# Optimization experiments

Hardware: AMD Instinct MI355X
Metric: run time of the kernel (lower is better)

Reference implementation:

```python
import jax, jax.numpy as jnp
import numpy as np

N = 50000
E = 800000
F_IN = 500
H = 5          # heads
C = 32         # per-head channels
HID = H * C    # 160
NC = 20        # num_classes
G = 8          # number of graphs in batch
SLOPE_ATT = 0.2   # GATConv attention leaky slope (PyG default)
SLOPE_ACT = 0.01  # F.leaky_relu default


def _layernorm(x, scale, bias, eps=1e-5):
    mu = jnp.mean(x, axis=-1, keepdims=True)
    var = jnp.var(x, axis=-1, keepdims=True)
    return (x - mu) * jax.lax.rsqrt(var + eps) * scale + bias


def _edge_softmax(logits, dst, num_nodes):
    # segment softmax over incoming edges of each destination node
    m = jax.ops.segment_max(logits, dst, num_segments=num_nodes)
    ex = jnp.exp(logits - m[dst])
    s = jax.ops.segment_sum(ex, dst, num_segments=num_nodes)
    return ex / (s[dst] + 1e-16)


def _gat_layer(x, src, dst, W, a_src, a_dst, b):
    n = x.shape[0]
    h = (x @ W).reshape(n, H, C)                       # [N,H,C]
    al_s = jnp.einsum('nhc,hc->nh', h, a_src)          # [N,H]
    al_d = jnp.einsum('nhc,hc->nh', h, a_dst)
    logits = jax.nn.leaky_relu(al_s[src] + al_d[dst], SLOPE_ATT)  # [Et,H]
    alpha = _edge_softmax(logits, dst, n)              # [Et,H]
    msg = h[src] * alpha[..., None]                    # [Et,H,C]
    out = jax.ops.segment_sum(msg, dst, num_segments=n).reshape(n, HID) + b
    return out, alpha


def setup_inputs():
    key = jax.random.key(0)
    ks = jax.random.split(key, 24)
    p = lambda k, shp: jax.random.normal(k, shp, jnp.float32) * 0.05
    x = jax.random.normal(ks[0], (N, F_IN), jnp.float32)
    edge_index = jax.random.randint(ks[1], (2, E), 0, N, jnp.int64)
    batch = jnp.sort(jax.random.randint(ks[2], (N,), 0, G, jnp.int64))
    return {
        'x': x, 'edge_index': edge_index, 'batch': batch,
        'W1': p(ks[3], (F_IN, HID)), 'a_src1': p(ks[4], (H, C)), 'a_dst1': p(ks[5], (H, C)), 'b1': jnp.zeros((HID,), jnp.float32),
        'ln1_s': jnp.ones((HID,), jnp.float32), 'ln1_b': jnp.zeros((HID,), jnp.float32),
        'W2': p(ks[6], (HID, HID)), 'a_src2': p(ks[7], (H, C)), 'a_dst2': p(ks[8], (H, C)), 'b2': jnp.zeros((HID,), jnp.float32),
        'ln2_s': jnp.ones((HID,), jnp.float32), 'ln2_b': jnp.zeros((HID,), jnp.float32),
        'Wm': p(ks[9], (HID, HID)), 'bm': jnp.zeros((HID,), jnp.float32),
        'Wmlp1': p(ks[10], (HID, HID)), 'bmlp1': jnp.zeros((HID,), jnp.float32),
        'ln3_s': jnp.ones((HID,), jnp.float32), 'ln3_b': jnp.zeros((HID,), jnp.float32),
        'Wmlp2': p(ks[11], (HID, NC)), 'bmlp2': jnp.zeros((NC,), jnp.float32),
    }


def reference(x, edge_index, batch, W1, a_src1, a_dst1, b1, ln1_s, ln1_b,
              W2, a_src2, a_dst2, b2, ln2_s, ln2_b, Wm, bm,
              Wmlp1, bmlp1, ln3_s, ln3_b, Wmlp2, bmlp2):
    n = x.shape[0]
    # PyG GATConv adds self-loops by default
    loops = jnp.arange(n, dtype=edge_index.dtype)
    src = jnp.concatenate([edge_index[0], loops])
    dst = jnp.concatenate([edge_index[1], loops])

    h1, alpha1 = _gat_layer(x, src, dst, W1, a_src1, a_dst1, b1)
    h1 = jax.nn.leaky_relu(h1, SLOPE_ACT)
    h1 = _layernorm(h1, ln1_s, ln1_b)      # dropout = identity at eval

    h2, alpha2 = _gat_layer(h1, src, dst, W2, a_src2, a_dst2, b2)
    h2 = jax.nn.leaky_relu(h2, SLOPE_ACT)
    h2 = _layernorm(h2, ln2_s, ln2_b)

    xo = jax.nn.leaky_relu(h2 @ Wm + bm, SLOPE_ACT)   # [N,HID]

    # global_mean_pool over batch assignment
    sums = jax.ops.segment_sum(xo, batch, num_segments=G)
    cnts = jax.ops.segment_sum(jnp.ones((n, 1), xo.dtype), batch, num_segments=G)
    pooled = sums / jnp.maximum(cnts, 1.0)            # [G,HID]

    z = pooled @ Wmlp1 + bmlp1
    z = jax.nn.relu(_layernorm(z, ln3_s, ln3_b))
    rec = z @ Wmlp2 + bmlp2                           # [G,NC]
    return xo, rec, alpha1, alpha2
```

## Files before the change

### kernel.cpp

```cpp
#include <hip/hip_runtime.h>
#include <hip/hip_bf16.h>
#include <cstdint>
#include <cstddef>

#define NN   50000
#define EE   800000
#define ET_  (EE + NN)
#define FIN  500
#define HID_ 160
#define NC_  20
#define GG   8

typedef __attribute__((ext_vector_type(8))) short ab8;
typedef __attribute__((ext_vector_type(4))) float f4;

static __device__ __forceinline__ unsigned short f2bf(float v) {
    union { float f; uint32_t u; } c; c.f = v;
    uint32_t r = c.u + 0x7FFFu + ((c.u >> 16) & 1u);
    return (unsigned short)(r >> 16);
}

static __device__ __forceinline__ int lbound_i(const int* arr, int n, int val) {
    int lo = 0, hi = n;
    while (lo < hi) { int mid = (lo + hi) >> 1; if (arr[mid] < val) lo = mid + 1; else hi = mid; }
    return lo;
}

__global__ __launch_bounds__(256) void k_hist(const int* __restrict__ ei, int* __restrict__ deg) {
    int e = blockIdx.x * 256 + threadIdx.x;
    if (e >= ET_) return;
    int d = (e < EE) ? ei[EE + e] : (e - EE);
    atomicAdd(&deg[d], 1);
}

__global__ __launch_bounds__(256) void k_scan1(const int* __restrict__ deg, int* __restrict__ rowptr,
                                               int* __restrict__ bsum) {
    __shared__ int s[256];
    int t = threadIdx.x;
    int base = blockIdx.x * 1024 + t * 4;
    int v0 = (base + 0 < NN) ? deg[base + 0] : 0;
    int v1 = (base + 1 < NN) ? deg[base + 1] : 0;
    int v2 = (base + 2 < NN) ? deg[base + 2] : 0;
    int v3 = (base + 3 < NN) ? deg[base + 3] : 0;
    int tot = v0 + v1 + v2 + v3;
    s[t] = tot;
    __syncthreads();
    for (int off = 1; off < 256; off <<= 1) {
        int y = (t >= off) ? s[t - off] : 0;
        __syncthreads();
        s[t] += y;
        __syncthreads();
    }
    int excl = s[t] - tot;
    if (t == 255) bsum[blockIdx.x] = s[255];
    if (base + 0 < NN) rowptr[base + 0] = excl;  excl += v0;
    if (base + 1 < NN) rowptr[base + 1] = excl;  excl += v1;
    if (base + 2 < NN) rowptr[base + 2] = excl;  excl += v2;
    if (base + 3 < NN) rowptr[base + 3] = excl;
}

__global__ void k_scan2(int* __restrict__ bsum, int nb) {
    int t = threadIdx.x;
    int v = (t < nb) ? bsum[t] : 0;
    int orig = v;
    for (int off = 1; off < 64; off <<= 1) {
        int y = __shfl_up(v, off);
        if (t >= off) v += y;
    }
    if (t < nb) bsum[t] = v - orig;
}

__global__ __launch_bounds__(256) void k_scan3(int* __restrict__ rowptr, const int* __restrict__ bsum,
                                               int* __restrict__ cursor) {
    int i = blockIdx.x * 256 + threadIdx.x;
    if (i < NN) {
        int r = rowptr[i] + bsum[i >> 10];
        rowptr[i] = r;
        cursor[i] = r;
    }
    if (i == NN) rowptr[NN] = ET_;
}

__global__ __launch_bounds__(256) void k_scatter(const int* __restrict__ ei, int* __restrict__ cursor,
                                                 int2* __restrict__ epair) {
    int e = blockIdx.x * 256 + threadIdx.x;
    if (e >= ET_) return;
    int s, d;
    if (e < EE) { s = ei[e]; d = ei[EE + e]; } else { s = e - EE; d = e - EE; }
    int slot = atomicAdd(&cursor[d], 1);
    epair[slot] = make_int2(e, s);
}

__global__ __launch_bounds__(256) void k_prep_w(const float* __restrict__ W, unsigned short* __restrict__ Wt,
                                                int K, int Kp) {
    int idx = blockIdx.x * 256 + threadIdx.x;
    if (idx >= HID_ * Kp) return;
    int n = idx / Kp, k = idx - n * Kp;
    float v = (k < K) ? W[(size_t)k * HID_ + n] : 0.f;
    Wt[idx] = f2bf(v);
}

__global__ __launch_bounds__(256) void k_gemm_mfma(const void* __restrict__ Av,
                                                   const unsigned short* __restrict__ Bt,
                                                   float* __restrict__ C, __hip_bfloat16* __restrict__ Cb,
                                                   int M, int K, int Kp, int a_bf16,
                                                   const float* __restrict__ bias, int act) {
    __shared__ __align__(16) unsigned short As[128 * 40];
    __shared__ __align__(16) unsigned short Bs[160 * 40];
    int tid  = threadIdx.x;
    int lane = tid & 63;
    int w    = tid >> 6;
    int fr   = lane & 15;
    int q8   = (lane >> 4) * 8;
    int row0 = blockIdx.x * 128;

    int arow  = tid >> 1;
    int abase = (tid & 1) * 16;

    f4 acc0[10], acc1[10];
#pragma unroll
    for (int t = 0; t < 10; t++) { acc0[t] = (f4)0.f; acc1[t] = (f4)0.f; }

    for (int k0 = 0; k0 < Kp; k0 += 32) {
        {
            int grow = row0 + arow;
            int bk = k0 + abase;
            if (a_bf16) {
                const unsigned short* Ab = (const unsigned short*)Av;
                ab8 v0 = (ab8)0, v1 = (ab8)0;
                if (grow < M) {
                    v0 = *reinterpret_cast<const ab8*>(&Ab[(size_t)grow * K + bk]);
                    v1 = *reinterpret_cast<const ab8*>(&Ab[(size_t)grow * K + bk + 8]);
                }
                *reinterpret_cast<ab8*>(&As[arow * 40 + abase])     = v0;
                *reinterpret_cast<ab8*>(&As[arow * 40 + abase + 8]) = v1;
            } else {
                const float* A = (const float*)Av;
                unsigned short pk[16];
                if (grow < M && bk + 16 <= K) {
                    const float4* src = reinterpret_cast<const float4*>(&A[(size_t)grow * K + bk]);
#pragma unroll
                    for (int f = 0; f < 4; f++) {
                        float4 v = src[f];
                        pk[f * 4 + 0] = f2bf(v.x); pk[f * 4 + 1] = f2bf(v.y);
                        pk[f * 4 + 2] = f2bf(v.z); pk[f * 4 + 3] = f2bf(v.w);
                    }
                } else {
#pragma unroll
                    for (int c = 0; c < 16; c++) {
                        int k = bk + c;
                        pk[c] = (grow < M && k < K) ? f2bf(A[(size_t)grow * K + k]) : (unsigned short)0;
                    }
                }
                *reinterpret_cast<ab8*>(&As[arow * 40 + abase])     = *reinterpret_cast<ab8*>(&pk[0]);
                *reinterpret_cast<ab8*>(&As[arow * 40 + abase + 8]) = *reinterpret_cast<ab8*>(&pk[8]);
            }
        }
        {
            for (int idx = tid; idx < 640; idx += 256) {
                int n = idx >> 2, c4 = (idx & 3) * 8;
                ab8 v = *reinterpret_cast<const ab8*>(&Bt[(size_t)n * Kp + k0 + c4]);
                *reinterpret_cast<ab8*>(&Bs[n * 40 + c4]) = v;
            }
        }
        __syncthreads();
        ab8 a0 = *reinterpret_cast<const ab8*>(&As[(w * 16 + fr) * 40 + q8]);
        ab8 a1 = *reinterpret_cast<const ab8*>(&As[(w * 16 + 64 + fr) * 40 + q8]);
#pragma unroll
        for (int t = 0; t < 10; t++) {
            ab8 b = *reinterpret_cast<const ab8*>(&Bs[(t * 16 + fr) * 40 + q8]);
            acc0[t] = __builtin_amdgcn_mfma_f32_16x16x32_bf16(a0, b, acc0[t], 0, 0, 0);
            acc1[t] = __builtin_amdgcn_mfma_f32_16x16x32_bf16(a1, b, acc1[t], 0, 0, 0);
        }
        __syncthreads();
    }
    int rbase0 = row0 + w * 16 + (lane >> 4) * 4;
#pragma unroll
    for (int t = 0; t < 10; t++) {
        int col = t * 16 + fr;
        float bv = bias ? bias[col] : 0.f;
#pragma unroll
        for (int i = 0; i < 4; i++) {
            int r0 = rbase0 + i;
            int r1 = r0 + 64;
            float v0 = acc0[t][i] + bv;
            float v1 = acc1[t][i] + bv;
            if (act) { v0 = v0 > 0.f ? v0 : 0.01f * v0; v1 = v1 > 0.f ? v1 : 0.01f * v1; }
            if (r0 < M) {
                if (C)  C[(size_t)r0 * HID_ + col] = v0;
                if (Cb) *reinterpret_cast<unsigned short*>(&Cb[(size_t)r0 * HID_ + col]) = f2bf(v0);
            }
            if (r1 < M) {
                if (C)  C[(size_t)r1 * HID_ + col] = v1;
                if (Cb) *reinterpret_cast<unsigned short*>(&Cb[(size_t)r1 * HID_ + col]) = f2bf(v1);
            }
        }
    }
}

__global__ __launch_bounds__(256) void k_node_att(const __hip_bfloat16* __restrict__ hmat,
                                                  const float* __restrict__ asrc, const float* __restrict__ adst,
                                                  float* __restrict__ als, float* __restrict__ ald) {
    int node = blockIdx.x * 4 + (threadIdx.x >> 6);
    int lane = threadIdx.x & 63;
    if (node >= NN) return;
    const __hip_bfloat16* row = &hmat[(size_t)node * HID_];
    float v0 = __bfloat162float(row[lane]);
    float v1 = __bfloat162float(row[lane + 64]);
    float s0 = v0 * asrc[lane],      d0 = v0 * adst[lane];
    float s1 = v1 * asrc[lane + 64], d1 = v1 * adst[lane + 64];
    float s2 = 0.f, d2 = 0.f;
    if (lane < 32) {
        float v2 = __bfloat162float(row[lane + 128]);
        s2 = v2 * asrc[lane + 128];
        d2 = v2 * adst[lane + 128];
    }
#pragma unroll
    for (int off = 16; off >= 1; off >>= 1) {
        s0 += __shfl_xor(s0, off); s1 += __shfl_xor(s1, off); s2 += __shfl_xor(s2, off);
        d0 += __shfl_xor(d0, off); d1 += __shfl_xor(d1, off); d2 += __shfl_xor(d2, off);
    }
    if (lane == 0) {
        als[node * 5 + 0] = s0; als[node * 5 + 2] = s1; als[node * 5 + 4] = s2;
        ald[node * 5 + 0] = d0; ald[node * 5 + 2] = d1; ald[node * 5 + 4] = d2;
    }
    if (lane == 32) {
        als[node * 5 + 1] = s0; als[node * 5 + 3] = s1;
        ald[node * 5 + 1] = d0; ald[node * 5 + 3] = d1;
    }
}

__global__ __launch_bounds__(256) void k_att_agg(const int* __restrict__ rowptr,
                                                 const int2* __restrict__ epair,
                                                 const float* __restrict__ als, const float* __restrict__ ald,
                                                 const __hip_bfloat16* __restrict__ hmat,
                                                 float* __restrict__ alphap,
                                                 float* __restrict__ alpha_out,
                                                 const float* __restrict__ bias,
                                                 const float* __restrict__ lns, const float* __restrict__ lnb,
                                                 __hip_bfloat16* __restrict__ outb) {
    __shared__ float sExp[4][64 * 5];
    __shared__ int2  sPair[4][64];
    int wv   = threadIdx.x >> 6;
    int lane = threadIdx.x & 63;
    int node = blockIdx.x * 4 + wv;
    if (node >= NN) return;
    int start = rowptr[node], end = rowptr[node + 1];
    int deg = end - start;
    bool fits = (deg <= 64);
    float ad[5];
#pragma unroll
    for (int h = 0; h < 5; h++) ad[h] = ald[node * 5 + h];

    float sm[5] = {0.f, 0.f, 0.f, 0.f, 0.f};
    for (int j = start + lane; j < end; j += 64) {
        int2 p = epair[j];
        const float* as = &als[(size_t)p.y * 5];
        int idx = j - start;
        if (fits) sPair[wv][idx] = p;
#pragma unroll
        for (int h = 0; h < 5; h++) {
            float l = as[h] + ad[h];
            l = l > 0.f ? l : 0.2f * l;
            float ex = __expf(fminf(l, 60.f));
            sm[h] += ex;
            if (fits) sExp[wv][idx * 5 + h] = ex;
            else      alphap[(size_t)j * 5 + h] = ex;
        }
    }
#pragma unroll
    for (int off = 32; off >= 1; off >>= 1)
#pragma unroll
        for (int h = 0; h < 5; h++) sm[h] += __shfl_xor(sm[h], off);
    float inv[5];
#pragma unroll
    for (int h = 0; h < 5; h++) inv[h] = 1.f / (sm[h] + 1e-16f);

    int h0 = lane >> 5;
    int h1 = h0 + 2;
    bool lo32 = lane < 32;
    float a0 = 0.f, a1 = 0.f, a2 = 0.f;
    float c0 = 0.f, c1 = 0.f, c2 = 0.f;

    if (fits) {
        if (lane < deg) {
            int2 p = sPair[wv][lane];
            float* ao = &alpha_out[(size_t)p.x * 5];
#pragma unroll
            for (int h = 0; h < 5; h++) ao[h] = sExp[wv][lane * 5 + h] * inv[h];
        }
        int idx = 0;
        for (; idx + 1 < deg; idx += 2) {
            int2 pA = sPair[wv][idx], pB = sPair[wv][idx + 1];
            float wA0 = sExp[wv][idx * 5 + h0] * inv[h0];
            float wA1 = sExp[wv][idx * 5 + h1] * inv[h1];
            float wB0 = sExp[wv][(idx + 1) * 5 + h0] * inv[h0];
            float wB1 = sExp[wv][(idx + 1) * 5 + h1] * inv[h1];
            const __hip_bfloat16* rA = &hmat[(size_t)pA.y * HID_];
            const __hip_bfloat16* rB = &hmat[(size_t)pB.y * HID_];
            float vA0 = __bfloat162float(rA[lane]);
            float vA1 = __bfloat162float(rA[lane + 64]);
            float vB0 = __bfloat162float(rB[lane]);
            float vB1 = __bfloat162float(rB[lane + 64]);
            a0 += wA0 * vA0; c0 += wB0 * vB0;
            a1 += wA1 * vA1; c1 += wB1 * vB1;
            if (lo32) {
                a2 += sExp[wv][idx * 5 + 4] * inv[4] * __bfloat162float(rA[lane + 128]);
                c2 += sExp[wv][(idx + 1) * 5 + 4] * inv[4] * __bfloat162float(rB[lane + 128]);
            }
        }
        if (idx < deg) {
            int2 p = sPair[wv][idx];
            float w0 = sExp[wv][idx * 5 + h0] * inv[h0];
            float w1 = sExp[wv][idx * 5 + h1] * inv[h1];
            const __hip_bfloat16* row = &hmat[(size_t)p.y * HID_];
            a0 += w0 * __bfloat162float(row[lane]);
            a1 += w1 * __bfloat162float(row[lane + 64]);
            if (lo32) a2 += sExp[wv][idx * 5 + 4] * inv[4] * __bfloat162float(row[lane + 128]);
        }
    } else {
        for (int j = start + lane; j < end; j += 64) {
            int2 p = epair[j];
            float* ao = &alpha_out[(size_t)p.x * 5];
#pragma unroll
            for (int h = 0; h < 5; h++) ao[h] = alphap[(size_t)j * 5 + h] * inv[h];
        }
        for (int j = start; j < end; j++) {
            int2 p = epair[j];
            const float* ap = &alphap[(size_t)j * 5];
            const __hip_bfloat16* row = &hmat[(size_t)p.y * HID_];
            a0 += ap[h0] * inv[h0] * __bfloat162float(row[lane]);
            a1 += ap[h1] * inv[h1] * __bfloat162float(row[lane + 64]);
            if (lo32) a2 += ap[4] * inv[4] * __bfloat162float(row[lane + 128]);
        }
    }
    a0 += c0; a1 += c1; a2 += c2;

    float v0 = a0 + bias[lane];       v0 = v0 > 0.f ? v0 : 0.01f * v0;
    float v1 = a1 + bias[lane + 64];  v1 = v1 > 0.f ? v1 : 0.01f * v1;
    float v2 = 0.f;
    if (lo32) { v2 = a2 + bias[lane + 128]; v2 = v2 > 0.f ? v2 : 0.01f * v2; }
    float s  = v0 + v1 + v2;
    float sq = v0 * v0 + v1 * v1 + v2 * v2;
#pragma unroll
    for (int off = 32; off >= 1; off >>= 1) {
        s  += __shfl_xor(s, off);
        sq += __shfl_xor(sq, off);
    }
    float m = s * (1.f / 160.f);
    float r = rsqrtf(sq * (1.f / 160.f) - m * m + 1e-5f);
    size_t ob = (size_t)node * HID_;
    outb[ob + lane]      = __hip_bfloat16_raw{f2bf((v0 - m) * r * lns[lane]      + lnb[lane])};
    outb[ob + lane + 64] = __hip_bfloat16_raw{f2bf((v1 - m) * r * lns[lane + 64] + lnb[lane + 64])};
    if (lo32)
        outb[ob + lane + 128] = __hip_bfloat16_raw{f2bf((v2 - m) * r * lns[lane + 128] + lnb[lane + 128])};
}

__global__ __launch_bounds__(192) void k_pool(const float* __restrict__ xo, const int* __restrict__ batch,
                                              float* __restrict__ pooled) {
    int g = blockIdx.x, chunk = blockIdx.y;
    int lo = lbound_i(batch, NN, g), hi = lbound_i(batch, NN, g + 1);
    int len = hi - lo;
    if (len <= 0) return;
    int per = (len + 31) / 32;
    int s = lo + chunk * per;
    int e = min(s + per, hi);
    if (s >= e) return;
    int ch = threadIdx.x;
    if (ch >= HID_) return;
    float acc = 0.f;
    for (int n = s; n < e; n++) acc += xo[(size_t)n * HID_ + ch];
    atomicAdd(&pooled[g * HID_ + ch], acc);
}

__global__ __launch_bounds__(256) void k_mlp(const float* __restrict__ pooled, const int* __restrict__ batch,
                                             const float* __restrict__ W1, const float* __restrict__ b1,
                                             const float* __restrict__ lns, const float* __restrict__ lnb,
                                             const float* __restrict__ W2, const float* __restrict__ b2,
                                             float* __restrict__ rec) {
    __shared__ float P[GG][HID_];
    __shared__ float Z[GG][HID_];
    __shared__ float mu[GG], rr[GG], ic[GG];
    int t = threadIdx.x;
    if (t < GG) {
        int lo = lbound_i(batch, NN, t), hi = lbound_i(batch, NN, t + 1);
        ic[t] = 1.f / fmaxf((float)(hi - lo), 1.f);
    }
    __syncthreads();
    for (int i = t; i < GG * HID_; i += 256) P[i / HID_][i % HID_] = pooled[i] * ic[i / HID_];
    __syncthreads();
    for (int i = t; i < GG * HID_; i += 256) {
        int g = i / HID_, j = i % HID_;
        float acc = b1[j];
        for (int k = 0; k < HID_; k++) acc += P[g][k] * W1[k * HID_ + j];
        Z[g][j] = acc;
    }
    __syncthreads();
    if (t < GG) {
        float s = 0.f, sq = 0.f;
        for (int k = 0; k < HID_; k++) { float z = Z[t][k]; s += z; sq += z * z; }
        float m = s / (float)HID_;
        mu[t] = m;
        rr[t] = rsqrtf(sq / (float)HID_ - m * m + 1e-5f);
    }
    __syncthreads();
    for (int i = t; i < GG * HID_; i += 256) {
        int g = i / HID_, j = i % HID_;
        float z = (Z[g][j] - mu[g]) * rr[g] * lns[j] + lnb[j];
        Z[g][j] = fmaxf(z, 0.f);
    }
    __syncthreads();
    for (int i = t; i < GG * NC_; i += 256) {
        int g = i / NC_, j = i % NC_;
        float acc = b2[j];
        for (int k = 0; k < HID_; k++) acc += Z[g][k] * W2[k * NC_ + j];
        rec[g * NC_ + j] = acc;
    }
}

extern "C" void kernel_launch(void* const* d_in, const int* in_sizes, int n_in,
                              void* d_out, int out_size, void* d_ws, size_t ws_size,
                              hipStream_t stream) {
    const float* x    = (const float*)d_in[0];
    const int*   ei   = (const int*)d_in[1];
    const int*   batch= (const int*)d_in[2];
    const float* W1   = (const float*)d_in[3];
    const float* as1  = (const float*)d_in[4];
    const float* ad1  = (const float*)d_in[5];
    const float* b1   = (const float*)d_in[6];
    const float* ln1s = (const float*)d_in[7];
    const float* ln1b = (const float*)d_in[8];
    const float* W2   = (const float*)d_in[9];
    const float* as2  = (const float*)d_in[10];
    const float* ad2  = (const float*)d_in[11];
    const float* b2   = (const float*)d_in[12];
    const float* ln2s = (const float*)d_in[13];
    const float* ln2b = (const float*)d_in[14];
    const float* Wm   = (const float*)d_in[15];
    const float* bm   = (const float*)d_in[16];
    const float* Wm1  = (const float*)d_in[17];
    const float* bm1  = (const float*)d_in[18];
    const float* ln3s = (const float*)d_in[19];
    const float* ln3b = (const float*)d_in[20];
    const float* Wm2  = (const float*)d_in[21];
    const float* bm2  = (const float*)d_in[22];

    float* out    = (float*)d_out;
    float* xo     = out;
    float* rec    = out + (size_t)NN * HID_;
    float* alpha1 = rec + GG * NC_;
    float* alpha2 = alpha1 + (size_t)ET_ * 5;

    char* w = (char*)d_ws;
    auto carve = [&](size_t bytes) { char* p = w; w += (bytes + 255) & ~(size_t)255; return p; };
    int*   deg    = (int*)carve((size_t)NN * 4);
    int*   rowptr = (int*)carve((size_t)(NN + 1) * 4);
    int*   cursor = (int*)carve((size_t)NN * 4);
    int2*  epair  = (int2*)carve((size_t)ET_ * 8);
    int*   bsum   = (int*)carve(64 * 4);
    __hip_bfloat16* hbuf  = (__hip_bfloat16*)carve((size_t)NN * HID_ * 2);
    __hip_bfloat16* xbufb = (__hip_bfloat16*)carve((size_t)NN * HID_ * 2);
    float* alphap = (float*)carve((size_t)ET_ * 5 * 4);
    float* als    = (float*)carve((size_t)NN * 5 * 4);
    float* ald    = (float*)carve((size_t)NN * 5 * 4);
    float* pooled = (float*)carve((size_t)GG * HID_ * 4);
    unsigned short* Wt1 = (unsigned short*)carve((size_t)HID_ * 512 * 2);
    unsigned short* Wt2 = (unsigned short*)carve((size_t)HID_ * HID_ * 2);
    unsigned short* Wmt = (unsigned short*)carve((size_t)HID_ * HID_ * 2);

    hipMemsetAsync(deg, 0, (size_t)NN * 4, stream);
    k_hist<<<(ET_ + 255) / 256, 256, 0, stream>>>(ei, deg);
    int nb = (NN + 1023) / 1024;
    k_scan1<<<nb, 256, 0, stream>>>(deg, rowptr, bsum);
    k_scan2<<<1, 64, 0, stream>>>(bsum, nb);
    k_scan3<<<(NN + 1 + 255) / 256, 256, 0, stream>>>(rowptr, bsum, cursor);
    k_scatter<<<(ET_ + 255) / 256, 256, 0, stream>>>(ei, cursor, epair);

    k_prep_w<<<(HID_ * 512 + 255) / 256, 256, 0, stream>>>(W1, Wt1, FIN, 512);
    k_prep_w<<<(HID_ * HID_ + 255) / 256, 256, 0, stream>>>(W2, Wt2, HID_, HID_);
    k_prep_w<<<(HID_ * HID_ + 255) / 256, 256, 0, stream>>>(Wm, Wmt, HID_, HID_);

    const int NWB = (NN + 3) / 4;
    const int GB  = (NN + 127) / 128;

    k_gemm_mfma<<<GB, 256, 0, stream>>>(x, Wt1, nullptr, hbuf, NN, FIN, 512, 0, nullptr, 0);
    k_node_att<<<NWB, 256, 0, stream>>>(hbuf, as1, ad1, als, ald);
    k_att_agg<<<NWB, 256, 0, stream>>>(rowptr, epair, als, ald, hbuf, alphap, alpha1,
                                       b1, ln1s, ln1b, xbufb);

    k_gemm_mfma<<<GB, 256, 0, stream>>>(xbufb, Wt2, nullptr, hbuf, NN, HID_, HID_, 1, nullptr, 0);
    k_node_att<<<NWB, 256, 0, stream>>>(hbuf, as2, ad2, als, ald);
    k_att_agg<<<NWB, 256, 0, stream>>>(rowptr, epair, als, ald, hbuf, alphap, alpha2,
                                       b2, ln2s, ln2b, xbufb);

    k_gemm_mfma<<<GB, 256, 0, stream>>>(xbufb, Wmt, xo, nullptr, NN, HID_, HID_, 1, bm, 1);
    hipMemsetAsync(pooled, 0, (size_t)GG * HID_ * 4, stream);
    k_pool<<<dim3(GG, 32), 192, 0, stream>>>(xo, batch, pooled);
    k_mlp<<<1, 256, 0, stream>>>(pooled, batch, Wm1, bm1, ln3s, ln3b, Wm2, bm2, rec);
}
```

Baseline: 673.8 us.

## Fuse attention dots and mean-pool into GEMM epilogue, vectorize aggregation loads

Computes the per-node attention logits (als/ald) inside the MFMA GEMM epilogue from fp32 accumulators, removing the separate k_node_att pass and its re-read of the bf16 feature matrix. It also folds the global mean-pool sums into the final GEMM's epilogue, using a block reduction when all 128 rows share a graph and per-element atomics otherwise, which removes k_pool and its re-read of xo. The three weight-prep launches are merged into one. The aggregation kernel now loads bf16 pairs as 32-bit words and writes packed outputs, cutting load instruction count. Attention logits now come from fp32 rather than bf16-rounded values, which changes numerics slightly.

```diff
diff --git a/kernel.cpp b/kernel.cpp
--- a/kernel.cpp
+++ b/kernel.cpp
@@ -18,6 +18,13 @@
     union { float f; uint32_t u; } c; c.f = v;
     uint32_t r = c.u + 0x7FFFu + ((c.u >> 16) & 1u);
     return (unsigned short)(r >> 16);
+}
+
+static __device__ __forceinline__ float2 bf2f2(uint32_t u) {
+    union { uint32_t u; float f; } a, b;
+    a.u = u << 16;
+    b.u = u & 0xffff0000u;
+    return make_float2(a.f, b.f);
 }
 
 static __device__ __forceinline__ int lbound_i(const int* arr, int n, int val) {
@@ -91,20 +98,33 @@
     epair[slot] = make_int2(e, s);
 }
 
-__global__ __launch_bounds__(256) void k_prep_w(const float* __restrict__ W, unsigned short* __restrict__ Wt,
-                                                int K, int Kp) {
+__global__ __launch_bounds__(256) void k_prep_all(const float* __restrict__ W1, unsigned short* __restrict__ Wt1,
+                                                  const float* __restrict__ W2, unsigned short* __restrict__ Wt2,
+                                                  const float* __restrict__ Wm, unsigned short* __restrict__ Wmt) {
     int idx = blockIdx.x * 256 + threadIdx.x;
-    if (idx >= HID_ * Kp) return;
-    int n = idx / Kp, k = idx - n * Kp;
-    float v = (k < K) ? W[(size_t)k * HID_ + n] : 0.f;
-    Wt[idx] = f2bf(v);
+    const int S1 = HID_ * 512, S2 = HID_ * HID_;
+    if (idx < S1) {
+        int n = idx / 512, k = idx - n * 512;
+        Wt1[idx] = (k < FIN) ? f2bf(W1[(size_t)k * HID_ + n]) : (unsigned short)0;
+    } else if (idx < S1 + S2) {
+        int j = idx - S1;
+        int n = j / HID_, k = j - n * HID_;
+        Wt2[j] = f2bf(W2[(size_t)k * HID_ + n]);
+    } else if (idx < S1 + 2 * S2) {
+        int j = idx - S1 - S2;
+        int n = j / HID_, k = j - n * HID_;
+        Wmt[j] = f2bf(Wm[(size_t)k * HID_ + n]);
+    }
 }
 
 __global__ __launch_bounds__(256) void k_gemm_mfma(const void* __restrict__ Av,
                                                    const unsigned short* __restrict__ Bt,
                                                    float* __restrict__ C, __hip_bfloat16* __restrict__ Cb,
                                                    int M, int K, int Kp, int a_bf16,
-                                                   const float* __restrict__ bias, int act) {
+                                                   const float* __restrict__ bias, int act,
+                                                   const float* __restrict__ asrc, const float* __restrict__ adst,
+                                                   float* __restrict__ als_o, float* __restrict__ ald_o,
+                                                   const int* __restrict__ batch_p, float* __restrict__ pooled) {
     __shared__ __align__(16) unsigned short As[128 * 40];
     __shared__ __align__(16) unsigned short Bs[160 * 40];
     int tid  = threadIdx.x;
@@ -174,7 +194,54 @@
         }
         __syncthreads();
     }
-    int rbase0 = row0 + w * 16 + (lane >> 4) * 4;
+
+    int q = lane >> 4;
+    if (als_o) {
+        float av_s[10], av_d[10];
+#pragma unroll
+        for (int t = 0; t < 10; t++) { av_s[t] = asrc[t * 16 + fr]; av_d[t] = adst[t * 16 + fr]; }
+#pragma unroll
+        for (int s = 0; s < 2; s++) {
+            const f4* ac = s ? acc1 : acc0;
+#pragma unroll
+            for (int i = 0; i < 4; i++) {
+                int r = row0 + w * 16 + q * 4 + i + s * 64;
+                float ps[5], pd[5];
+#pragma unroll
+                for (int h = 0; h < 5; h++) {
+                    ps[h] = ac[2 * h][i] * av_s[2 * h] + ac[2 * h + 1][i] * av_s[2 * h + 1];
+                    pd[h] = ac[2 * h][i] * av_d[2 * h] + ac[2 * h + 1][i] * av_d[2 * h + 1];
+                }
+#pragma unroll
+                for (int off = 8; off >= 1; off >>= 1)
+#pragma unroll
+                    for (int h = 0; h < 5; h++) {
+                        ps[h] += __shfl_xor(ps[h], off);
+                        pd[h] += __shfl_xor(pd[h], off);
+                    }
+                if (fr == 0 && r < M) {
+#pragma unroll
+                    for (int h = 0; h < 5; h++) {
+                        als_o[(size_t)r * 5 + h] = ps[h];
+                        ald_o[(size_t)r * 5 + h] = pd[h];
+                    }
+                }
+            }
+        }
+    }
+
+    int gu = -2;
+    if (pooled) {
+        int gl = batch_p[row0];
+        int rhi = row0 + 127; if (rhi >= M) rhi = M - 1;
+        int gh = batch_p[rhi];
+        gu = (gl == gh) ? gl : -1;
+    }
+    float psum[10];
+#pragma unroll
+    for (int t = 0; t < 10; t++) psum[t] = 0.f;
+
+    int rbase0 = row0 + w * 16 + q * 4;
 #pragma unroll
     for (int t = 0; t < 10; t++) {
         int col = t * 16 + fr;
@@ -194,39 +261,26 @@
                 if (C)  C[(size_t)r1 * HID_ + col] = v1;
                 if (Cb) *reinterpret_cast<unsigned short*>(&Cb[(size_t)r1 * HID_ + col]) = f2bf(v1);
             }
-        }
-    }
-}
-
-__global__ __launch_bounds__(256) void k_node_att(const __hip_bfloat16* __restrict__ hmat,
-                                                  const float* __restrict__ asrc, const float* __restrict__ adst,
-                                                  float* __restrict__ als, float* __restrict__ ald) {
-    int node = blockIdx.x * 4 + (threadIdx.x >> 6);
-    int lane = threadIdx.x & 63;
-    if (node >= NN) return;
-    const __hip_bfloat16* row = &hmat[(size_t)node * HID_];
-    float v0 = __bfloat162float(row[lane]);
-    float v1 = __bfloat162float(row[lane + 64]);
-    float s0 = v0 * asrc[lane],      d0 = v0 * adst[lane];
-    float s1 = v1 * asrc[lane + 64], d1 = v1 * adst[lane + 64];
-    float s2 = 0.f, d2 = 0.f;
-    if (lane < 32) {
-        float v2 = __bfloat162float(row[lane + 128]);
-        s2 = v2 * asrc[lane + 128];
-        d2 = v2 * adst[lane + 128];
-    }
-#pragma unroll
-    for (int off = 16; off >= 1; off >>= 1) {
-        s0 += __shfl_xor(s0, off); s1 += __shfl_xor(s1, off); s2 += __shfl_xor(s2, off);
-        d0 += __shfl_xor(d0, off); d1 += __shfl_xor(d1, off); d2 += __shfl_xor(d2, off);
-    }
-    if (lane == 0) {
-        als[node * 5 + 0] = s0; als[node * 5 + 2] = s1; als[node * 5 + 4] = s2;
-        ald[node * 5 + 0] = d0; ald[node * 5 + 2] = d1; ald[node * 5 + 4] = d2;
-    }
-    if (lane == 32) {
-        als[node * 5 + 1] = s0; als[node * 5 + 3] = s1;
-        ald[node * 5 + 1] = d0; ald[node * 5 + 3] = d1;
+            if (gu >= 0) {
+                if (r0 < M) psum[t] += v0;
+                if (r1 < M) psum[t] += v1;
+            } else if (gu == -1) {
+                if (r0 < M) atomicAdd(&pooled[batch_p[r0] * HID_ + col], v0);
+                if (r1 < M) atomicAdd(&pooled[batch_p[r1] * HID_ + col], v1);
+            }
+        }
+    }
+    if (gu >= 0) {
+#pragma unroll
+        for (int t = 0; t < 10; t++) {
+            psum[t] += __shfl_xor(psum[t], 16);
+            psum[t] += __shfl_xor(psum[t], 32);
+        }
+        if (q == 0) {
+#pragma unroll
+            for (int t = 0; t < 10; t++)
+                atomicAdd(&pooled[gu * HID_ + t * 16 + fr], psum[t]);
+        }
     }
 }
 
@@ -276,11 +330,12 @@
 #pragma unroll
     for (int h = 0; h < 5; h++) inv[h] = 1.f / (sm[h] + 1e-16f);
 
-    int h0 = lane >> 5;
-    int h1 = h0 + 2;
-    bool lo32 = lane < 32;
-    float a0 = 0.f, a1 = 0.f, a2 = 0.f;
-    float c0 = 0.f, c1 = 0.f, c2 = 0.f;
+    int h0 = lane >> 4;
+    bool lo16 = lane < 16;
+    int c01 = 2 * lane;
+    int c2  = 128 + 2 * lane;
+    float2 A  = make_float2(0.f, 0.f), B2 = make_float2(0.f, 0.f);
+    float2 A2 = make_float2(0.f, 0.f), B22 = make_float2(0.f, 0.f);
 
     if (fits) {
         if (lane < deg) {
@@ -291,32 +346,35 @@
         }
         int idx = 0;
         for (; idx + 1 < deg; idx += 2) {
-            int2 pA = sPair[wv][idx], pB = sPair[wv][idx + 1];
-            float wA0 = sExp[wv][idx * 5 + h0] * inv[h0];
-            float wA1 = sExp[wv][idx * 5 + h1] * inv[h1];
-            float wB0 = sExp[wv][(idx + 1) * 5 + h0] * inv[h0];
-            float wB1 = sExp[wv][(idx + 1) * 5 + h1] * inv[h1];
-            const __hip_bfloat16* rA = &hmat[(size_t)pA.y * HID_];
-            const __hip_bfloat16* rB = &hmat[(size_t)pB.y * HID_];
-            float vA0 = __bfloat162float(rA[lane]);
-            float vA1 = __bfloat162float(rA[lane + 64]);
-            float vB0 = __bfloat162float(rB[lane]);
-            float vB1 = __bfloat162float(rB[lane + 64]);
-            a0 += wA0 * vA0; c0 += wB0 * vB0;
-            a1 += wA1 * vA1; c1 += wB1 * vB1;
-            if (lo32) {
-                a2 += sExp[wv][idx * 5 + 4] * inv[4] * __bfloat162float(rA[lane + 128]);
-                c2 += sExp[wv][(idx + 1) * 5 + 4] * inv[4] * __bfloat162float(rB[lane + 128]);
+            int sA = sPair[wv][idx].y, sB = sPair[wv][idx + 1].y;
+            float wA = sExp[wv][idx * 5 + h0] * inv[h0];
+            float wB = sExp[wv][(idx + 1) * 5 + h0] * inv[h0];
+            const unsigned short* rA = (const unsigned short*)&hmat[(size_t)sA * HID_];
+            const unsigned short* rB = (const unsigned short*)&hmat[(size_t)sB * HID_];
+            float2 fA = bf2f2(*reinterpret_cast<const uint32_t*>(&rA[c01]));
+            float2 fB = bf2f2(*reinterpret_cast<const uint32_t*>(&rB[c01]));
+            A.x += wA * fA.x; A.y += wA * fA.y;
+            B2.x += wB * fB.x; B2.y += wB * fB.y;
+            if (lo16) {
+                float wA4 = sExp[wv][idx * 5 + 4] * inv[4];
+                float wB4 = sExp[wv][(idx + 1) * 5 + 4] * inv[4];
+                float2 gA = bf2f2(*reinterpret_cast<const uint32_t*>(&rA[c2]));
+                float2 gB = bf2f2(*reinterpret_cast<const uint32_t*>(&rB[c2]));
+                A2.x += wA4 * gA.x; A2.y += wA4 * gA.y;
+                B22.x += wB4 * gB.x; B22.y += wB4 * gB.y;
             }
         }
         if (idx < deg) {
-            int2 p = sPair[wv][idx];
-            float w0 = sExp[wv][idx * 5 + h0] * inv[h0];
-            float w1 = sExp[wv][idx * 5 + h1] * inv[h1];
-            const __hip_bfloat16* row = &hmat[(size_t)p.y * HID_];
-            a0 += w0 * __bfloat162float(row[lane]);
-            a1 += w1 * __bfloat162float(row[lane + 64]);
-            if (lo32) a2 += sExp[wv][idx * 5 + 4] * inv[4] * __bfloat162float(row[lane + 128]);
+            int sA = sPair[wv][idx].y;
+            float wA = sExp[wv][idx * 5 + h0] * inv[h0];
+            const unsigned short* rA = (const unsigned short*)&hmat[(size_t)sA * HID_];
+            float2 fA = bf2f2(*reinterpret_cast<const uint32_t*>(&rA[c01]));
+            A.x += wA * fA.x; A.y += wA * fA.y;
+            if (lo16) {
+                float wA4 = sExp[wv][idx * 5 + 4] * inv[4];
+                float2 gA = bf2f2(*reinterpret_cast<const uint32_t*>(&rA[c2]));
+                A2.x += wA4 * gA.x; A2.y += wA4 * gA.y;
+            }
         }
     } else {
         for (int j = start + lane; j < end; j += 64) {
@@ -328,20 +386,30 @@
         for (int j = start; j < end; j++) {
             int2 p = epair[j];
             const float* ap = &alphap[(size_t)j * 5];
-            const __hip_bfloat16* row = &hmat[(size_t)p.y * HID_];
-            a0 += ap[h0] * inv[h0] * __bfloat162float(row[lane]);
-            a1 += ap[h1] * inv[h1] * __bfloat162float(row[lane + 64]);
-            if (lo32) a2 += ap[4] * inv[4] * __bfloat162float(row[lane + 128]);
-        }
-    }
-    a0 += c0; a1 += c1; a2 += c2;
-
-    float v0 = a0 + bias[lane];       v0 = v0 > 0.f ? v0 : 0.01f * v0;
-    float v1 = a1 + bias[lane + 64];  v1 = v1 > 0.f ? v1 : 0.01f * v1;
-    float v2 = 0.f;
-    if (lo32) { v2 = a2 + bias[lane + 128]; v2 = v2 > 0.f ? v2 : 0.01f * v2; }
-    float s  = v0 + v1 + v2;
-    float sq = v0 * v0 + v1 * v1 + v2 * v2;
+            float wA = ap[h0] * inv[h0];
+            const unsigned short* rA = (const unsigned short*)&hmat[(size_t)p.y * HID_];
+            float2 fA = bf2f2(*reinterpret_cast<const uint32_t*>(&rA[c01]));
+            A.x += wA * fA.x; A.y += wA * fA.y;
+            if (lo16) {
+                float wA4 = ap[4] * inv[4];
+                float2 gA = bf2f2(*reinterpret_cast<const uint32_t*>(&rA[c2]));
+                A2.x += wA4 * gA.x; A2.y += wA4 * gA.y;
+            }
+        }
+    }
+    A.x += B2.x; A.y += B2.y; A2.x += B22.x; A2.y += B22.y;
+
+    float2 bb = *reinterpret_cast<const float2*>(&bias[c01]);
+    float v0 = A.x + bb.x;  v0 = v0 > 0.f ? v0 : 0.01f * v0;
+    float v1 = A.y + bb.y;  v1 = v1 > 0.f ? v1 : 0.01f * v1;
+    float v2 = 0.f, v3 = 0.f;
+    if (lo16) {
+        float2 b2 = *reinterpret_cast<const float2*>(&bias[c2]);
+        v2 = A2.x + b2.x; v2 = v2 > 0.f ? v2 : 0.01f * v2;
+        v3 = A2.y + b2.y; v3 = v3 > 0.f ? v3 : 0.01f * v3;
+    }
+    float s  = v0 + v1 + v2 + v3;
+    float sq = v0 * v0 + v1 * v1 + v2 * v2 + v3 * v3;
 #pragma unroll
     for (int off = 32; off >= 1; off >>= 1) {
         s  += __shfl_xor(s, off);
@@ -350,27 +418,20 @@
     float m = s * (1.f / 160.f);
     float r = rsqrtf(sq * (1.f / 160.f) - m * m + 1e-5f);
     size_t ob = (size_t)node * HID_;
-    outb[ob + lane]      = __hip_bfloat16_raw{f2bf((v0 - m) * r * lns[lane]      + lnb[lane])};
-    outb[ob + lane + 64] = __hip_bfloat16_raw{f2bf((v1 - m) * r * lns[lane + 64] + lnb[lane + 64])};
-    if (lo32)
-        outb[ob + lane + 128] = __hip_bfloat16_raw{f2bf((v2 - m) * r * lns[lane + 128] + lnb[lane + 128])};
-}
-
-__global__ __launch_bounds__(192) void k_pool(const float* __restrict__ xo, const int* __restrict__ batch,
-                                              float* __restrict__ pooled) {
-    int g = blockIdx.x, chunk = blockIdx.y;
-    int lo = lbound_i(batch, NN, g), hi = lbound_i(batch, NN, g + 1);
-    int len = hi - lo;
-    if (len <= 0) return;
-    int per = (len + 31) / 32;
-    int s = lo + chunk * per;
-    int e = min(s + per, hi);
-    if (s >= e) return;
-    int ch = threadIdx.x;
-    if (ch >= HID_) return;
-    float acc = 0.f;
-    for (int n = s; n < e; n++) acc += xo[(size_t)n * HID_ + ch];
-    atomicAdd(&pooled[g * HID_ + ch], acc);
+    {
+        float2 sc = *reinterpret_cast<const float2*>(&lns[c01]);
+        float2 bi = *reinterpret_cast<const float2*>(&lnb[c01]);
+        uint32_t pk = (uint32_t)f2bf((v0 - m) * r * sc.x + bi.x)
+                    | ((uint32_t)f2bf((v1 - m) * r * sc.y + bi.y) << 16);
+        *reinterpret_cast<uint32_t*>(&outb[ob + c01]) = pk;
+    }
+    if (lo16) {
+        float2 sc = *reinterpret_cast<const float2*>(&lns[c2]);
+        float2 bi = *reinterpret_cast<const float2*>(&lnb[c2]);
+        uint32_t pk = (uint32_t)f2bf((v2 - m) * r * sc.x + bi.x)
+                    | ((uint32_t)f2bf((v3 - m) * r * sc.y + bi.y) << 16);
+        *reinterpret_cast<uint32_t*>(&outb[ob + c2]) = pk;
+    }
 }
 
 __global__ __launch_bounds__(256) void k_mlp(const float* __restrict__ pooled, const int* __restrict__ batch,
@@ -476,25 +537,24 @@
     k_scan3<<<(NN + 1 + 255) / 256, 256, 0, stream>>>(rowptr, bsum, cursor);
     k_scatter<<<(ET_ + 255) / 256, 256, 0, stream>>>(ei, cursor, epair);
 
-    k_prep_w<<<(HID_ * 512 + 255) / 256, 256, 0, stream>>>(W1, Wt1, FIN, 512);
-    k_prep_w<<<(HID_ * HID_ + 255) / 256, 256, 0, stream>>>(W2, Wt2, HID_, HID_);
-    k_prep_w<<<(HID_ * HID_ + 255) / 256, 256, 0, stream>>>(Wm, Wmt, HID_, HID_);
+    const int PREP = HID_ * 512 + 2 * HID_ * HID_;
+    k_prep_all<<<(PREP + 255) / 256, 256, 0, stream>>>(W1, Wt1, W2, Wt2, Wm, Wmt);
+    hipMemsetAsync(pooled, 0, (size_t)GG * HID_ * 4, stream);
 
     const int NWB = (NN + 3) / 4;
     const int GB  = (NN + 127) / 128;
 
-    k_gemm_mfma<<<GB, 256, 0, stream>>>(x, Wt1, nullptr, hbuf, NN, FIN, 512, 0, nullptr, 0);
-    k_node_att<<<NWB, 256, 0, stream>>>(hbuf, as1, ad1, als, ald);
+    k_gemm_mfma<<<GB, 256, 0, stream>>>(x, Wt1, nullptr, hbuf, NN, FIN, 512, 0, nullptr, 0,
+                                        as1, ad1, als, ald, nullptr, nullptr);
     k_att_agg<<<NWB, 256, 0, stream>>>(rowptr, epair, als, ald, hbuf, alphap, alpha1,
                                        b1, ln1s, ln1b, xbufb);
 
-    k_gemm_mfma<<<GB, 256, 0, stream>>>(xbufb, Wt2, nullptr, hbuf, NN, HID_, HID_, 1, nullptr, 0);
-    k_node_att<<<NWB, 256, 0, stream>>>(hbuf, as2, ad2, als, ald);
+    k_gemm_mfma<<<GB, 256, 0, stream>>>(xbufb, Wt2, nullptr, hbuf, NN, HID_, HID_, 1, nullptr, 0,
+                                        as2, ad2, als, ald, nullptr, nullptr);
     k_att_agg<<<NWB, 256, 0, stream>>>(rowptr, epair, als, ald, hbuf, alphap, alpha2,
                                        b2, ln2s, ln2b, xbufb);
 
-    k_gemm_mfma<<<GB, 256, 0, stream>>>(xbufb, Wmt, xo, nullptr, NN, HID_, HID_, 1, bm, 1);
-    hipMemsetAsync(pooled, 0, (size_t)GG * HID_ * 4, stream);
-    k_pool<<<dim3(GG, 32), 192, 0, stream>>>(xo, batch, pooled);
+    k_gemm_mfma<<<GB, 256, 0, stream>>>(xbufb, Wmt, xo, nullptr, NN, HID_, HID_, 1, bm, 1,
+                                        nullptr, nullptr, nullptr, nullptr, batch, pooled);
     k_mlp<<<1, 256, 0, stream>>>(pooled, batch, Wm1, bm1, ln3s, ln3b, Wm2, bm2, rec);
 }
```

Result: no change. 665.4 us (-1.3%).
